# Kernel optimization log

Hardware: AMD Instinct MI355X
Metric: run time of the kernel (lower is better)

Reference implementation:

```python
import jax, jax.numpy as jnp
import numpy as np


def _gather_tree(step_ids, parent_ids, max_seq_lens, end_token):
    """Vectorized beam-search backtrace.

    step_ids, parent_ids: [max_len, batch, beam] int32
    max_seq_lens: [batch] int32
    Returns beams: [max_len, batch, beam]
    """
    max_len, batch, beam = step_ids.shape
    # current back-pointer per (batch, beam); starts at own beam index
    own = jnp.broadcast_to(jnp.arange(beam, dtype=step_ids.dtype), (batch, beam))
    msl = jnp.minimum(max_seq_lens, max_len)[:, None]  # [batch, 1]

    def step(cur, xs):
        t, s_t, p_t = xs  # s_t, p_t: [batch, beam]
        active = t < msl  # [batch, 1] -> broadcasts over beam
        tok = jnp.where(active, jnp.take_along_axis(s_t, cur, axis=1), end_token)
        new_cur = jnp.where(active, jnp.take_along_axis(p_t, cur, axis=1), cur)
        return new_cur, tok

    ts = jnp.arange(max_len - 1, -1, -1, dtype=msl.dtype)
    _, toks = jax.lax.scan(step, own, (ts, step_ids[::-1], parent_ids[::-1]))
    beams = toks[::-1]  # [max_len, batch, beam]
    # once an end_token is produced, every later position becomes end_token
    ended = jnp.cumsum((beams == end_token).astype(jnp.int32), axis=0) > 0
    return jnp.where(ended, jnp.asarray(end_token, beams.dtype), beams)


def setup_inputs() -> dict:
    key = jax.random.key(0)
    k1, k2, k3 = jax.random.split(key, 3)
    max_len, batch, beam = 256, 4096, 8
    output_ids = jax.random.randint(k1, (max_len, batch, beam), 0, 32000, dtype=jnp.int32)
    parent_ids = jax.random.randint(k2, (max_len, batch, beam), 0, beam, dtype=jnp.int32)
    out_seq_lens = jax.random.randint(k3, (batch, beam), 0, max_len, dtype=jnp.int32)
    return {
        "output_ids": output_ids,
        "parent_ids": parent_ids,
        "out_seq_lens": out_seq_lens,
        "end_id": 2,
    }


def reference(output_ids, parent_ids, out_seq_lens, end_id):
    # finalize(): per-batch max decode length over beams
    max_lens = jnp.max(out_seq_lens, axis=1)  # [batch]
    ids = _gather_tree(output_ids, parent_ids, max_lens, end_id)  # [max_len, batch, beam]
    ids = jnp.transpose(ids, (1, 2, 0))  # einsum 'ijk->jki' -> [batch, beam, max_len]
    lengths = jnp.sum((ids != end_id).astype(output_ids.dtype), axis=-1)  # [batch, beam]
    return ids, lengths
```

## Files before the change

kernel.cpp:

```cpp
#include <hip/hip_runtime.h>


constexpr int MAX_LEN = 256;
constexpr int BATCH   = 4096;
constexpr int BEAM    = 8;
constexpr int NCHAIN  = BATCH * BEAM;
constexpr int PITCH   = 65;
constexpr int NW      = 16;
constexpr int SEG     = 16;

__global__ __launch_bounds__(1024)
void gather_tree_kernel(const int* __restrict__ step_ids,
                        const int* __restrict__ parent_ids,
                        const int* __restrict__ seq_lens,
                        const int* __restrict__ end_id_p,
                        int* __restrict__ out_ids,
                        int* __restrict__ out_lens)
{
    __shared__ int      s_tile[MAX_LEN * PITCH];
    __shared__ unsigned hist[NW * 2 * 64];
    __shared__ unsigned segmap[NW * 8];
    __shared__ int      fe_buf[NW * 64];

    const int tid   = threadIdx.x;
    const int w     = tid >> 6;
    const int lane  = tid & 63;
    const int b_loc = lane >> 3;
    const int h     = lane & 7;
    const int bj0   = blockIdx.x * 64;
    const int tbase = w * SEG;
    const int end_tok = *end_id_p;

    int sl = seq_lens[bj0 + lane];
    sl = max(sl, __shfl_xor(sl, 1));
    sl = max(sl, __shfl_xor(sl, 2));
    sl = max(sl, __shfl_xor(sl, 4));
    const int msl = min(sl, MAX_LEN);

    int cur = h;
    for (int kb = SEG - 8; kb >= 0; kb -= 8) {
        unsigned hw = 0;
        #pragma unroll
        for (int i = 7; i >= 0; --i) {
            const int t = tbase + kb + i;
            const int g = t * NCHAIN + bj0 + lane;
            int s = step_ids[g];
            int p = parent_ids[g];
            s_tile[t * PITCH + lane] = s;
            int pg = __shfl(p, b_loc * 8 + cur);
            hw |= (unsigned)cur << (3 * i);
            cur = (t < msl) ? (pg & 7) : cur;
        }
        hist[(w * 2 + (kb >> 3)) * 64 + lane] = hw;
    }
    unsigned fm = (unsigned)cur << (3 * h);
    fm |= (unsigned)__shfl_xor((int)fm, 1);
    fm |= (unsigned)__shfl_xor((int)fm, 2);
    fm |= (unsigned)__shfl_xor((int)fm, 4);
    if (h == 0) segmap[w * 8 + b_loc] = fm;

    __syncthreads();

    int e = h;
    for (int ww = NW - 1; ww > w; --ww)
        e = (segmap[ww * 8 + b_loc] >> (3 * e)) & 7;

    int fe = MAX_LEN;
    for (int kb = 0; kb < SEG; kb += 8) {
        const unsigned hw = hist[(w * 2 + (kb >> 3)) * 64 + b_loc * 8 + e];
        #pragma unroll
        for (int i = 0; i < 8; ++i) {
            const int t = tbase + kb + i;
            const int c = (hw >> (3 * i)) & 7;
            int tok = s_tile[t * PITCH + b_loc * 8 + c];
            tok = (t < msl) ? tok : end_tok;
            if (tok == end_tok) fe = min(fe, t);
            s_tile[t * PITCH + lane] = tok;
        }
    }
    fe_buf[w * 64 + lane] = fe;

    __syncthreads();

    int feg = fe_buf[lane];
    #pragma unroll
    for (int w2 = 1; w2 < NW; ++w2) feg = min(feg, fe_buf[w2 * 64 + lane]);
    if (w == 0) out_lens[bj0 + lane] = feg;

    #pragma unroll
    for (int cc = 0; cc < 4; ++cc) {
        const int c = w * 4 + cc;
        const int fec = __shfl(feg, c);
        #pragma unroll
        for (int k = 0; k < 4; ++k) {
            const int t = k * 64 + lane;
            const int v = s_tile[t * PITCH + c];
            out_ids[(bj0 + c) * MAX_LEN + t] = (t < fec) ? v : end_tok;
        }
    }
}

extern "C" void kernel_launch(void* const* d_in, const int* in_sizes, int n_in,
                              void* d_out, int out_size, void* d_ws, size_t ws_size,
                              hipStream_t stream)
{
    const int* step_ids   = (const int*)d_in[0];
    const int* parent_ids = (const int*)d_in[1];
    const int* seq_lens   = (const int*)d_in[2];
    const int* end_id     = (const int*)d_in[3];

    int* out_ids  = (int*)d_out;
    int* out_lens = (int*)d_out + MAX_LEN * NCHAIN;

    gather_tree_kernel<<<NCHAIN / 64, 1024, 0, stream>>>(
        step_ids, parent_ids, seq_lens, end_id, out_ids, out_lens);
}
```

Baseline: 105.1 us.

## Pack parent pointers into per-step LDS maps and defer token loads to pass two

Parent ids are now read with int4 vector loads and packed into 24-bit per-(step, batch) permutation maps in shared memory. The first backward walk then uses only these compact maps instead of shuffling full parent values. Step ids are no longer staged in shared memory in pass one. Pass two reads them directly from global memory and selects the token via shuffle, writing into a transposed tile so the output copy reads along contiguous time. The goals are to cut LDS traffic and the serial shuffle dependency, but step ids are now loaded in the second phase after a barrier, which may expose global latency.

Result: slower. 109.2 us (+4.0%).

```diff
diff --git a/kernel.cpp b/kernel.cpp
--- a/kernel.cpp
+++ b/kernel.cpp
@@ -5,11 +5,12 @@
 constexpr int BATCH   = 4096;
 constexpr int BEAM    = 8;
 constexpr int NCHAIN  = BATCH * BEAM;
-constexpr int PITCH   = 65;
 constexpr int NW      = 16;
 constexpr int SEG     = 16;
+constexpr int TP      = 257;
+constexpr unsigned ID_MAP = 0xFAC688u;
 
-__global__ __launch_bounds__(1024)
+__global__ __launch_bounds__(1024, 8)
 void gather_tree_kernel(const int* __restrict__ step_ids,
                         const int* __restrict__ parent_ids,
                         const int* __restrict__ seq_lens,
@@ -17,8 +18,8 @@
                         int* __restrict__ out_ids,
                         int* __restrict__ out_lens)
 {
-    __shared__ int      s_tile[MAX_LEN * PITCH];
-    __shared__ unsigned hist[NW * 2 * 64];
+    __shared__ int      tile2[64 * TP];
+    __shared__ unsigned maps[MAX_LEN * 8];
     __shared__ unsigned segmap[NW * 8];
     __shared__ int      fe_buf[NW * 64];
 
@@ -37,21 +38,28 @@
     sl = max(sl, __shfl_xor(sl, 4));
     const int msl = min(sl, MAX_LEN);
 
+    {
+        const int t_sub = lane >> 4;
+        const int q     = lane & 15;
+        const int4* p4  = (const int4*)parent_ids;
+        #pragma unroll
+        for (int k = 0; k < SEG; k += 4) {
+            const int t = tbase + k + t_sub;
+            int4 p = p4[t * (NCHAIN / 4) + (bj0 >> 2) + q];
+            unsigned mm = (unsigned)(p.x & 7)        | ((unsigned)(p.y & 7) << 3)
+                        | ((unsigned)(p.z & 7) << 6) | ((unsigned)(p.w & 7) << 9);
+            unsigned oo = (unsigned)__shfl_xor((int)mm, 1);
+            if ((q & 1) == 0)
+                maps[t * 8 + (q >> 1)] = mm | (oo << 12);
+        }
+    }
+
     int cur = h;
-    for (int kb = SEG - 8; kb >= 0; kb -= 8) {
-        unsigned hw = 0;
-        #pragma unroll
-        for (int i = 7; i >= 0; --i) {
-            const int t = tbase + kb + i;
-            const int g = t * NCHAIN + bj0 + lane;
-            int s = step_ids[g];
-            int p = parent_ids[g];
-            s_tile[t * PITCH + lane] = s;
-            int pg = __shfl(p, b_loc * 8 + cur);
-            hw |= (unsigned)cur << (3 * i);
-            cur = (t < msl) ? (pg & 7) : cur;
-        }
-        hist[(w * 2 + (kb >> 3)) * 64 + lane] = hw;
+    #pragma unroll
+    for (int i = SEG - 1; i >= 0; --i) {
+        const int t = tbase + i;
+        const unsigned m = (t < msl) ? maps[t * 8 + b_loc] : ID_MAP;
+        cur = (m >> (3 * cur)) & 7;
     }
     unsigned fm = (unsigned)cur << (3 * h);
     fm |= (unsigned)__shfl_xor((int)fm, 1);
@@ -66,17 +74,17 @@
         e = (segmap[ww * 8 + b_loc] >> (3 * e)) & 7;
 
     int fe = MAX_LEN;
-    for (int kb = 0; kb < SEG; kb += 8) {
-        const unsigned hw = hist[(w * 2 + (kb >> 3)) * 64 + b_loc * 8 + e];
-        #pragma unroll
-        for (int i = 0; i < 8; ++i) {
-            const int t = tbase + kb + i;
-            const int c = (hw >> (3 * i)) & 7;
-            int tok = s_tile[t * PITCH + b_loc * 8 + c];
-            tok = (t < msl) ? tok : end_tok;
-            if (tok == end_tok) fe = min(fe, t);
-            s_tile[t * PITCH + lane] = tok;
-        }
+    int c2 = e;
+    #pragma unroll
+    for (int i = SEG - 1; i >= 0; --i) {
+        const int t = tbase + i;
+        const int tok_own = step_ids[t * NCHAIN + bj0 + lane];
+        const int tokg = __shfl(tok_own, b_loc * 8 + c2);
+        const unsigned m = (t < msl) ? maps[t * 8 + b_loc] : ID_MAP;
+        const int tok = (t < msl) ? tokg : end_tok;
+        if (tok == end_tok) fe = min(fe, t);
+        tile2[lane * TP + t] = tok;
+        c2 = (m >> (3 * c2)) & 7;
     }
     fe_buf[w * 64 + lane] = fe;
 
@@ -94,7 +102,7 @@
         #pragma unroll
         for (int k = 0; k < 4; ++k) {
             const int t = k * 64 + lane;
-            const int v = s_tile[t * PITCH + c];
+            const int v = tile2[c * TP + t];
             out_ids[(bj0 + c) * MAX_LEN + t] = (t < fec) ? v : end_tok;
         }
     }
```
